# Optimization experiments

Measured on AMD Instinct MI355X. Metric: run time of the kernel, lower is better.

Reference implementation:

```python
import jax, jax.numpy as jnp
import numpy as np

H = 16      # num_heads
D = 64      # head_dim
HS = H * D  # hidden_size
B = 8
S = 1024


def setup_inputs() -> dict:
    key = jax.random.key(0)
    ks = jax.random.split(key, 12)
    scale = 1.0 / np.sqrt(HS)
    inp = {
        "v": jax.random.normal(ks[0], (B, S, HS), jnp.float32),
        "k": jax.random.normal(ks[1], (B, S, HS), jnp.float32),
        "q": jax.random.normal(ks[2], (B, S, HS), jnp.float32),
        "mask": jax.random.randint(ks[3], (B, 1, 1, S), 0, 2).astype(bool),
        "Wq": jax.random.normal(ks[4], (HS, HS), jnp.float32) * scale,
        "bq": jnp.zeros((HS,), jnp.float32),
        "Wk": jax.random.normal(ks[5], (HS, HS), jnp.float32) * scale,
        "bk": jnp.zeros((HS,), jnp.float32),
        "Wv": jax.random.normal(ks[6], (HS, HS), jnp.float32) * scale,
        "bv": jnp.zeros((HS,), jnp.float32),
        "Wo": jax.random.normal(ks[7], (HS, HS), jnp.float32) * scale,
        "bo": jnp.zeros((HS,), jnp.float32),
    }
    return inp


def _split_heads(x):
    b, s, _ = x.shape
    return x.reshape(b, s, H, D).transpose(0, 2, 1, 3)  # [B,H,S,D]


def reference(v, k, q, mask, Wq, bq, Wk, bk, Wv, bv, Wo, bo):
    # torch Linear: y = x @ W.T + b
    qh = _split_heads(q @ Wq.T + bq)
    kh = _split_heads(k @ Wk.T + bk)
    vh = _split_heads(v @ Wv.T + bv)
    scores = jnp.einsum("bhqd,bhkd->bhqk", qh, kh) / jnp.sqrt(jnp.float32(D))
    scores = jnp.where(mask, jnp.float32(-1e9), scores)
    att = jax.nn.softmax(scores, axis=-1)
    out = jnp.einsum("bhqk,bhkd->bhqd", att, vh)  # [B,H,S,D]
    out = out.transpose(0, 2, 1, 3).reshape(v.shape[0], -1, HS)
    return out @ Wo.T + bo
```

## Files before the change

### kernel.cpp

```cpp
#include <hip/hip_runtime.h>
#include <hip/hip_bf16.h>

#define HH   16
#define DD   64
#define HSZ  1024
#define BB   8
#define SS   1024
#define NTOK (BB*SS)
#define LOG2E 1.4426950408889634f
#define NCVTB 2048

typedef __attribute__((ext_vector_type(8))) short bf16x8;
typedef __attribute__((ext_vector_type(4))) float f32x4;
typedef unsigned short u16;
typedef __attribute__((ext_vector_type(4))) unsigned short u16x4;

__device__ __forceinline__ u16 bfc(float x) {
    __hip_bfloat16 h = __float2bfloat16(x);
    return *(u16*)&h;
}

__device__ __forceinline__ float exp2fast(float x) {
    return __builtin_amdgcn_exp2f(x);
}

__device__ __forceinline__ void gload16(const u16* g, u16* l) {
    __builtin_amdgcn_global_load_lds(
        (const __attribute__((address_space(1))) void*)g,
        (__attribute__((address_space(3))) void*)l, 16, 0, 0);
}

__device__ __forceinline__ void mask_scan_body(const void* mask,
                                               int* __restrict__ rmap,
                                               int* __restrict__ Larr, int b) {
    const int tid = threadIdx.x;
    const unsigned char* mball = (const unsigned char*)mask;

    __shared__ int fmt_s;
    __shared__ int wtot[4];
    __shared__ int Ls;
    if (tid == 0) fmt_s = 0;
    __syncthreads();
    int nz = 0;
    for (int i = tid; i < BB * SS; i += 256)
        if ((i & 3) && mball[i]) nz = 1;
    if (nz) fmt_s = 1;
    __syncthreads();
    const int fmt = fmt_s;

    const int base = tid * 4;
    int v[4];
#pragma unroll
    for (int e = 0; e < 4; ++e) {
        int val = fmt ? (int)mball[(size_t)b * SS + base + e]
                      : ((const int*)mask)[(size_t)b * SS + base + e];
        v[e] = (val == 0) ? 1 : 0;
    }
    int ts = v[0] + v[1] + v[2] + v[3];

    const int lane = tid & 63, wv = tid >> 6;
    int incl = ts;
#pragma unroll
    for (int d = 1; d < 64; d <<= 1) {
        int t = __shfl_up(incl, d);
        if (lane >= d) incl += t;
    }
    if (lane == 63) wtot[wv] = incl;
    __syncthreads();
    int woff = 0;
    for (int w = 0; w < wv; ++w) woff += wtot[w];
    int run = woff + incl - ts;
#pragma unroll
    for (int e = 0; e < 4; ++e) {
        if (v[e]) rmap[(size_t)b * SS + run] = base + e;
        run += v[e];
    }
    __syncthreads();
    if (tid == 0) {
        Ls = wtot[0] + wtot[1] + wtot[2] + wtot[3];
        Larr[b] = Ls;
    }
    __syncthreads();
    for (int j = Ls + tid; j < SS; j += 256) rmap[(size_t)b * SS + j] = 0;
}

__global__ __launch_bounds__(256) void cvt_scan_kernel(
        const float* __restrict__ q,  u16* __restrict__ dq,
        const float* __restrict__ k,  u16* __restrict__ dk,
        const float* __restrict__ v,  u16* __restrict__ dv,
        const float* __restrict__ w0, u16* __restrict__ dw0,
        const float* __restrict__ w1, u16* __restrict__ dw1,
        const float* __restrict__ w2, u16* __restrict__ dw2,
        const float* __restrict__ w3, u16* __restrict__ dw3,
        const void* mask, int* __restrict__ rmap, int* __restrict__ Larr) {
    if (blockIdx.x >= NCVTB) {
        mask_scan_body(mask, rmap, Larr, blockIdx.x - NCVTB);
        return;
    }
    const int NX = NTOK * HSZ / 8;
    const int NW = HSZ * HSZ / 8;
    const int ntot = 3 * NX + 4 * NW;
    int i = blockIdx.x * blockDim.x + threadIdx.x;
    const int stride = NCVTB * 256;
    for (; i < ntot; i += stride) {
        const float* s; u16* d; int j = i;
        if      (j < NX)            { s = q;  d = dq;  }
        else if ((j -= NX) < NX)    { s = k;  d = dk;  }
        else if ((j -= NX) < NX)    { s = v;  d = dv;  }
        else if ((j -= NX) < NW)    { s = w0; d = dw0; }
        else if ((j -= NW) < NW)    { s = w1; d = dw1; }
        else if ((j -= NW) < NW)    { s = w2; d = dw2; }
        else    { j -= NW;            s = w3; d = dw3; }
        f32x4 a = *(const f32x4*)&s[(size_t)j * 8];
        f32x4 b = *(const f32x4*)&s[(size_t)j * 8 + 4];
        union { bf16x8 v8; u16 u[8]; } t;
#pragma unroll
        for (int e = 0; e < 4; ++e) { t.u[e] = bfc(a[e]); t.u[4 + e] = bfc(b[e]); }
        *(bf16x8*)&d[(size_t)j * 8] = t.v8;
    }
}

template<int MODE>
__device__ __forceinline__ void proj_body(const u16* __restrict__ X,
                                          const u16* __restrict__ W,
                                          const float* __restrict__ bias,
                                          const int* __restrict__ rmap,
                                          const int* __restrict__ Larr,
                                          void* __restrict__ Yv,
                                          u16* Xs0, u16* Ws0,
                                          u16* Xs1, u16* Ws1) {
    const int bm = blockIdx.x;
    const int bn = blockIdx.y;
    const int tid  = threadIdx.x;
    const int wave = tid >> 6;
    const int lane = tid & 63;
    const int l15  = lane & 15;
    const int g    = lane >> 4;
    const int wr   = wave >> 1;
    const int wc   = wave & 1;

    const int b_   = bm >> 3;
    const int row0 = (bm & 7) * 128;
    if constexpr (MODE == 1 || MODE == 2) {
        const int L = Larr[b_];
        const int Lpad = ((L + 127) >> 7) << 7;
        if (row0 >= Lpad) return;
    }

    f32x4 acc[4][4] = {};

    int srow[4], scol[4], xr[4];
#pragma unroll
    for (int i = 0; i < 4; ++i) {
        const int slot = wave * 256 + i * 64 + lane;
        const int r = slot >> 3, s = slot & 7;
        srow[i] = r;
        scol[i] = (s ^ (r & 7)) * 8;
        if constexpr (MODE == 1 || MODE == 2)
            xr[i] = (b_ << 10) + rmap[(size_t)b_ * SS + row0 + r];
        else
            xr[i] = bm * 128 + r;
    }

    auto stage = [&](u16* Xd, u16* Wd, int k0) {
#pragma unroll
        for (int i = 0; i < 4; ++i) {
            gload16(&X[(size_t)xr[i] * HSZ + k0 + scol[i]], &Xd[(wave * 4 + i) * 512]);
            gload16(&W[(size_t)(bn * 128 + srow[i]) * HSZ + k0 + scol[i]],
                    &Wd[(wave * 4 + i) * 512]);
        }
    };
    auto compute = [&](const u16* Xc, const u16* Wc) {
#pragma unroll
        for (int kk = 0; kk < 2; ++kk) {
            const int cw = ((kk * 4 + g) ^ (l15 & 7)) * 8;
            bf16x8 a[4], bb[4];
#pragma unroll
            for (int m = 0; m < 4; ++m)
                a[m] = *(const bf16x8*)&Xc[(size_t)(wr * 64 + m * 16 + l15) * 64 + cw];
#pragma unroll
            for (int n = 0; n < 4; ++n)
                bb[n] = *(const bf16x8*)&Wc[(size_t)(wc * 64 + n * 16 + l15) * 64 + cw];
#pragma unroll
            for (int m = 0; m < 4; ++m)
#pragma unroll
                for (int n = 0; n < 4; ++n)
                    acc[m][n] = __builtin_amdgcn_mfma_f32_16x16x32_bf16(a[m], bb[n], acc[m][n], 0, 0, 0);
        }
    };

    stage(Xs0, Ws0, 0);
    __syncthreads();
    const int NT = HSZ / 64;
    for (int t = 0; t < NT; ++t) {
        const int p = t & 1;
        if (t + 1 < NT) stage(p ? Xs0 : Xs1, p ? Ws0 : Ws1, (t + 1) * 64);
        compute(p ? Xs1 : Xs0, p ? Ws1 : Ws0);
        __syncthreads();
    }

#pragma unroll
    for (int m = 0; m < 4; ++m) {
#pragma unroll
        for (int n = 0; n < 4; ++n) {
            const int o = bn * 128 + wc * 64 + n * 16 + l15;
            const float bvv = bias[o];
            const int h_ = o >> 6, d = o & 63;
#pragma unroll
            for (int r = 0; r < 4; ++r) {
                const int lrow = wr * 64 + m * 16 + g * 4 + r;
                float y = acc[m][n][r] + bvv;
                if constexpr (MODE == 0) {
                    const int nrow = bm * 128 + lrow;
                    int bb_ = nrow >> 10, s = nrow & 1023;
                    ((u16*)Yv)[(((size_t)bb_ * HH + h_) * SS + s) * DD + d] = bfc(y * (0.125f * LOG2E));
                } else if constexpr (MODE == 1) {
                    ((u16*)Yv)[(((size_t)b_ * HH + h_) * SS + row0 + lrow) * DD + d] = bfc(y);
                } else if constexpr (MODE == 2) {
                    ((u16*)Yv)[(((size_t)b_ * HH + h_) * DD + d) * SS + row0 + lrow] = bfc(y);
                } else {
                    const int nrow = bm * 128 + lrow;
                    ((float*)Yv)[(size_t)nrow * HSZ + o] = y;
                }
            }
        }
    }
}

__global__ __launch_bounds__(256) void proj_qkv_kernel(
        const u16* __restrict__ qbf, const u16* __restrict__ wqb,
        const float* __restrict__ bq, u16* __restrict__ Qh,
        const u16* __restrict__ kbf, const u16* __restrict__ wkb,
        const float* __restrict__ bk, u16* __restrict__ Kh,
        const u16* __restrict__ vbf, const u16* __restrict__ wvb,
        const float* __restrict__ bv, u16* __restrict__ Vt,
        const int* __restrict__ rmap, const int* __restrict__ Larr) {
    __shared__ u16 Xs0[128 * 64], Ws0[128 * 64];
    __shared__ u16 Xs1[128 * 64], Ws1[128 * 64];
    if (blockIdx.z == 0)
        proj_body<0>(qbf, wqb, bq, rmap, Larr, Qh, Xs0, Ws0, Xs1, Ws1);
    else if (blockIdx.z == 1)
        proj_body<1>(kbf, wkb, bk, rmap, Larr, Kh, Xs0, Ws0, Xs1, Ws1);
    else
        proj_body<2>(vbf, wvb, bv, rmap, Larr, Vt, Xs0, Ws0, Xs1, Ws1);
}

__global__ __launch_bounds__(256) void proj_o_kernel(
        const u16* __restrict__ X, const u16* __restrict__ W,
        const float* __restrict__ bias, const int* __restrict__ rmap,
        const int* __restrict__ Larr, float* __restrict__ out) {
    __shared__ u16 Xs0[128 * 64], Ws0[128 * 64];
    __shared__ u16 Xs1[128 * 64], Ws1[128 * 64];
    proj_body<3>(X, W, bias, rmap, Larr, out, Xs0, Ws0, Xs1, Ws1);
}

__global__ __launch_bounds__(256, 2) void attn_kernel(const u16* __restrict__ Qh,
                                                      const u16* __restrict__ Kh,
                                                      const u16* __restrict__ Vt,
                                                      const int* __restrict__ Larr,
                                                      u16* __restrict__ ctx) {
    const int qt = blockIdx.x;
    const int h  = blockIdx.y;
    const int b  = blockIdx.z;
    const int bh = b * HH + h;

    const int tid  = threadIdx.x;
    const int wave = tid >> 6;
    const int lane = tid & 63;
    const int l15  = lane & 15;
    const int g    = lane >> 4;
    const int qw0  = qt * 256 + wave * 64;

    __shared__ u16 Ks[2][64 * 64];
    __shared__ u16 Vs[2][64 * 64];
    __shared__ u16 Pw[4][2][16][72];

    const u16* Qb = Qh + ((size_t)bh * SS + qw0) * DD;
    const u16* Kb = Kh + (size_t)bh * SS * DD;
    const u16* Vb = Vt + (size_t)bh * DD * SS;

    const int L = Larr[b];
    const int nchunks = (L + 63) >> 6;

    bf16x8 qf[4][2];
#pragma unroll
    for (int qq = 0; qq < 4; ++qq)
#pragma unroll
        for (int hh = 0; hh < 2; ++hh)
            qf[qq][hh] = *(const bf16x8*)&Qb[(size_t)(qq * 16 + l15) * DD + hh * 32 + g * 8];

    f32x4 o[4][4] = {};
    float mrun[4] = { -3e38f, -3e38f, -3e38f, -3e38f };
    float lrun[4] = { 0.0f, 0.0f, 0.0f, 0.0f };

    auto stage = [&](u16* Kp, u16* Vp, int c0) {
#pragma unroll
        for (int i = 0; i < 2; ++i) {
            const int slot = i * 256 + tid;
            const int r  = slot >> 3;
            const int cs = ((slot & 7) ^ (r & 7)) * 8;
            u16* dstK = Kp + (size_t)(i * 256 + wave * 64) * 8;
            u16* dstV = Vp + (size_t)(i * 256 + wave * 64) * 8;
            gload16(&Kb[(size_t)(c0 + r) * DD + cs], dstK);
            gload16(&Vb[(size_t)r * SS + c0 + cs],   dstV);
        }
    };
    auto loadKfrag = [&](const u16* Kp, bf16x8 (&kf)[8]) {
#pragma unroll
        for (int kt = 0; kt < 4; ++kt)
#pragma unroll
            for (int hh = 0; hh < 2; ++hh) {
                const int cw = ((hh * 4 + g) ^ (l15 & 7)) * 8;
                kf[kt * 2 + hh] = *(const bf16x8*)&Kp[(size_t)(kt * 16 + l15) * 64 + cw];
            }
    };
    auto loadVfrag = [&](const u16* Vp, bf16x8 (&vf)[8]) {
#pragma unroll
        for (int dt = 0; dt < 4; ++dt)
#pragma unroll
            for (int kh = 0; kh < 2; ++kh) {
                const int cw = ((kh * 4 + g) ^ (l15 & 7)) * 8;
                vf[dt * 2 + kh] = *(const bf16x8*)&Vp[(size_t)(dt * 16 + l15) * 64 + cw];
            }
    };

    auto process = [&](const bf16x8 (&kf)[8], const bf16x8 (&vf)[8], int c0) {
#pragma unroll
        for (int qq = 0; qq < 4; ++qq) {
            f32x4 s[4];
#pragma unroll
            for (int kt = 0; kt < 4; ++kt) {
                f32x4 a = {};
                a = __builtin_amdgcn_mfma_f32_16x16x32_bf16(kf[kt * 2 + 0], qf[qq][0], a, 0, 0, 0);
                a = __builtin_amdgcn_mfma_f32_16x16x32_bf16(kf[kt * 2 + 1], qf[qq][1], a, 0, 0, 0);
                s[kt] = a;
            }
            if (c0 + 64 > L) {
#pragma unroll
                for (int kt = 0; kt < 4; ++kt) {
                    const int kid = c0 + kt * 16 + g * 4;
#pragma unroll
                    for (int r = 0; r < 4; ++r)
                        s[kt][r] = (kid + r < L) ? s[kt][r] : -3e38f;
                }
            }
            float pmk[4];
#pragma unroll
            for (int kt = 0; kt < 4; ++kt)
                pmk[kt] = fmaxf(fmaxf(s[kt][0], s[kt][1]), fmaxf(s[kt][2], s[kt][3]));
            float pm = fmaxf(fmaxf(pmk[0], pmk[1]), fmaxf(pmk[2], pmk[3]));
            pm = fmaxf(pm, __shfl_xor(pm, 16));
            pm = fmaxf(pm, __shfl_xor(pm, 32));

            if (!__all(pm <= mrun[qq] + 11.5416f)) {
                float sc = exp2fast(mrun[qq] - pm);
                mrun[qq] = pm;
                lrun[qq] *= sc;
                float f0 = __shfl(sc, g * 4 + 0);
                float f1 = __shfl(sc, g * 4 + 1);
                float f2 = __shfl(sc, g * 4 + 2);
                float f3 = __shfl(sc, g * 4 + 3);
#pragma unroll
                for (int dt = 0; dt < 4; ++dt) {
                    o[qq][dt][0] *= f0; o[qq][dt][1] *= f1;
                    o[qq][dt][2] *= f2; o[qq][dt][3] *= f3;
                }
            }

            float ls = 0.0f;
#pragma unroll
            for (int kt = 0; kt < 4; ++kt) {
                union { u16x4 v; u16 u[4]; } pv;
#pragma unroll
                for (int r = 0; r < 4; ++r) {
                    float e = exp2fast(s[kt][r] - mrun[qq]);
                    ls += e;
                    pv.u[r] = bfc(e);
                }
                *(u16x4*)&Pw[wave][qq & 1][l15][kt * 16 + g * 4] = pv.v;
            }
            ls += __shfl_xor(ls, 16);
            ls += __shfl_xor(ls, 32);
            lrun[qq] += ls;

#pragma unroll
            for (int kh = 0; kh < 2; ++kh) {
                bf16x8 pa = *(const bf16x8*)&Pw[wave][qq & 1][l15][kh * 32 + g * 8];
#pragma unroll
                for (int dt = 0; dt < 4; ++dt)
                    o[qq][dt] = __builtin_amdgcn_mfma_f32_16x16x32_bf16(pa, vf[dt * 2 + kh], o[qq][dt], 0, 0, 0);
            }
        }
    };

    stage(&Ks[0][0], &Vs[0][0], 0);
    __syncthreads();
    for (int c = 0; c < nchunks; ++c) {
        const int p = c & 1;
        if (c + 1 < nchunks) stage(&Ks[p ^ 1][0], &Vs[p ^ 1][0], (c + 1) * 64);
        bf16x8 kf[8], vf[8];
        loadKfrag(&Ks[p][0], kf);
        loadVfrag(&Vs[p][0], vf);
        process(kf, vf, c * 64);
        __syncthreads();
    }

#pragma unroll
    for (int qq = 0; qq < 4; ++qq) {
        float inv = 1.0f / lrun[qq];
        float i0 = __shfl(inv, g * 4 + 0);
        float i1 = __shfl(inv, g * 4 + 1);
        float i2 = __shfl(inv, g * 4 + 2);
        float i3 = __shfl(inv, g * 4 + 3);
#pragma unroll
        for (int dt = 0; dt < 4; ++dt) {
            const int col = h * DD + dt * 16 + l15;
            const int qr  = b * SS + qw0 + qq * 16 + g * 4;
            ctx[(size_t)(qr + 0) * HSZ + col] = bfc(o[qq][dt][0] * i0);
            ctx[(size_t)(qr + 1) * HSZ + col] = bfc(o[qq][dt][1] * i1);
            ctx[(size_t)(qr + 2) * HSZ + col] = bfc(o[qq][dt][2] * i2);
            ctx[(size_t)(qr + 3) * HSZ + col] = bfc(o[qq][dt][3] * i3);
        }
    }
}

extern "C" void kernel_launch(void* const* d_in, const int* in_sizes, int n_in,
                              void* d_out, int out_size, void* d_ws, size_t ws_size,
                              hipStream_t stream) {
    const float* v    = (const float*)d_in[0];
    const float* k    = (const float*)d_in[1];
    const float* q    = (const float*)d_in[2];
    const void*  mask = d_in[3];
    const float* Wq = (const float*)d_in[4];
    const float* bq = (const float*)d_in[5];
    const float* Wk = (const float*)d_in[6];
    const float* bk = (const float*)d_in[7];
    const float* Wv = (const float*)d_in[8];
    const float* bv = (const float*)d_in[9];
    const float* Wo = (const float*)d_in[10];
    const float* bo = (const float*)d_in[11];

    u16* qbf = (u16*)d_out;
    u16* kbf = qbf + (size_t)NTOK * HSZ;

    char* ws = (char*)d_ws;
    int*   rmap = (int*)ws;
    int*   Larr = (int*)(ws + 32768);
    u16*   wqb  = (u16*)(ws + 65536);
    u16*   wkb  = wqb + (size_t)HSZ * HSZ;
    u16*   wvb  = wkb + (size_t)HSZ * HSZ;
    u16*   wob  = wvb + (size_t)HSZ * HSZ;
    u16*   vbf  = wob + (size_t)HSZ * HSZ;
    u16*   Qh   = vbf + (size_t)NTOK * HSZ;
    u16*   Kh   = Qh + (size_t)NTOK * HSZ;
    u16*   Vt   = Kh + (size_t)NTOK * HSZ;
    u16*   ctx  = vbf;

    cvt_scan_kernel<<<NCVTB + BB, 256, 0, stream>>>(q, qbf, k, kbf, v, vbf,
                                                    Wq, wqb, Wk, wkb, Wv, wvb, Wo, wob,
                                                    mask, rmap, Larr);

    dim3 pgrid(NTOK / 128, HSZ / 128, 3);
    proj_qkv_kernel<<<pgrid, 256, 0, stream>>>(qbf, wqb, bq, Qh,
                                               kbf, wkb, bk, Kh,
                                               vbf, wvb, bv, Vt,
                                               rmap, Larr);

    dim3 agrid(SS / 256, HH, BB);
    attn_kernel<<<agrid, 256, 0, stream>>>(Qh, Kh, Vt, Larr, ctx);

    dim3 ogrid(NTOK / 128, HSZ / 128);
    proj_o_kernel<<<ogrid, 256, 0, stream>>>(ctx, wob, bo, rmap, Larr, (float*)d_out);
}
```

Baseline: 158.0 us.

## Shrink projection GEMM K-tile to 32 with paired-row swizzled LDS layout

The projection GEMM now stages 32-wide K slices instead of 64. Each pair of rows is packed into one 64-element LDS row with an XOR swizzle, and the fragment loads are remapped to match. This halves LDS use per block, which may let more blocks share a CU and hide latency. In exchange there are twice as many pipeline iterations and barriers per tile, and fewer MFMAs between each sync.

```diff
diff --git a/kernel.cpp b/kernel.cpp
--- a/kernel.cpp
+++ b/kernel.cpp
@@ -149,52 +149,54 @@
 
     f32x4 acc[4][4] = {};
 
-    int srow[4], scol[4], xr[4];
-#pragma unroll
-    for (int i = 0; i < 4; ++i) {
-        const int slot = wave * 256 + i * 64 + lane;
-        const int r = slot >> 3, s = slot & 7;
-        srow[i] = r;
-        scol[i] = (s ^ (r & 7)) * 8;
+    int xrow[2], wrow[2], scol[2];
+#pragma unroll
+    for (int i = 0; i < 2; ++i) {
+        const int slot = wave * 128 + i * 64 + lane;
+        const int sr = slot >> 3, qs = slot & 7;
+        const int p  = qs ^ (sr & 7);
+        const int r  = 2 * sr + (p >> 2);
+        scol[i] = (p & 3) * 8;
+        wrow[i] = bn * 128 + r;
         if constexpr (MODE == 1 || MODE == 2)
-            xr[i] = (b_ << 10) + rmap[(size_t)b_ * SS + row0 + r];
+            xrow[i] = (b_ << 10) + rmap[(size_t)b_ * SS + row0 + r];
         else
-            xr[i] = bm * 128 + r;
+            xrow[i] = bm * 128 + r;
     }
 
     auto stage = [&](u16* Xd, u16* Wd, int k0) {
 #pragma unroll
-        for (int i = 0; i < 4; ++i) {
-            gload16(&X[(size_t)xr[i] * HSZ + k0 + scol[i]], &Xd[(wave * 4 + i) * 512]);
-            gload16(&W[(size_t)(bn * 128 + srow[i]) * HSZ + k0 + scol[i]],
-                    &Wd[(wave * 4 + i) * 512]);
+        for (int i = 0; i < 2; ++i) {
+            gload16(&X[(size_t)xrow[i] * HSZ + k0 + scol[i]], &Xd[(wave * 2 + i) * 512]);
+            gload16(&W[(size_t)wrow[i] * HSZ + k0 + scol[i]], &Wd[(wave * 2 + i) * 512]);
         }
     };
     auto compute = [&](const u16* Xc, const u16* Wc) {
-#pragma unroll
-        for (int kk = 0; kk < 2; ++kk) {
-            const int cw = ((kk * 4 + g) ^ (l15 & 7)) * 8;
-            bf16x8 a[4], bb[4];
-#pragma unroll
-            for (int m = 0; m < 4; ++m)
-                a[m] = *(const bf16x8*)&Xc[(size_t)(wr * 64 + m * 16 + l15) * 64 + cw];
+        const int qoff = ((((l15 & 1) << 2) + g) ^ (l15 >> 1)) * 8;
+        bf16x8 a[4], bb[4];
+#pragma unroll
+        for (int m = 0; m < 4; ++m) {
+            const int sr = wr * 32 + m * 8 + (l15 >> 1);
+            a[m] = *(const bf16x8*)&Xc[(size_t)sr * 64 + qoff];
+        }
+#pragma unroll
+        for (int n = 0; n < 4; ++n) {
+            const int sr = wc * 32 + n * 8 + (l15 >> 1);
+            bb[n] = *(const bf16x8*)&Wc[(size_t)sr * 64 + qoff];
+        }
+#pragma unroll
+        for (int m = 0; m < 4; ++m)
 #pragma unroll
             for (int n = 0; n < 4; ++n)
-                bb[n] = *(const bf16x8*)&Wc[(size_t)(wc * 64 + n * 16 + l15) * 64 + cw];
-#pragma unroll
-            for (int m = 0; m < 4; ++m)
-#pragma unroll
-                for (int n = 0; n < 4; ++n)
-                    acc[m][n] = __builtin_amdgcn_mfma_f32_16x16x32_bf16(a[m], bb[n], acc[m][n], 0, 0, 0);
-        }
+                acc[m][n] = __builtin_amdgcn_mfma_f32_16x16x32_bf16(a[m], bb[n], acc[m][n], 0, 0, 0);
     };
 
     stage(Xs0, Ws0, 0);
     __syncthreads();
-    const int NT = HSZ / 64;
+    const int NT = HSZ / 32;
     for (int t = 0; t < NT; ++t) {
         const int p = t & 1;
-        if (t + 1 < NT) stage(p ? Xs0 : Xs1, p ? Ws0 : Ws1, (t + 1) * 64);
+        if (t + 1 < NT) stage(p ? Xs0 : Xs1, p ? Ws0 : Ws1, (t + 1) * 32);
         compute(p ? Xs1 : Xs0, p ? Ws1 : Ws0);
         __syncthreads();
     }
@@ -235,8 +237,8 @@
         const u16* __restrict__ vbf, const u16* __restrict__ wvb,
         const float* __restrict__ bv, u16* __restrict__ Vt,
         const int* __restrict__ rmap, const int* __restrict__ Larr) {
-    __shared__ u16 Xs0[128 * 64], Ws0[128 * 64];
-    __shared__ u16 Xs1[128 * 64], Ws1[128 * 64];
+    __shared__ u16 Xs0[128 * 32], Ws0[128 * 32];
+    __shared__ u16 Xs1[128 * 32], Ws1[128 * 32];
     if (blockIdx.z == 0)
         proj_body<0>(qbf, wqb, bq, rmap, Larr, Qh, Xs0, Ws0, Xs1, Ws1);
     else if (blockIdx.z == 1)
@@ -249,8 +251,8 @@
         const u16* __restrict__ X, const u16* __restrict__ W,
         const float* __restrict__ bias, const int* __restrict__ rmap,
         const int* __restrict__ Larr, float* __restrict__ out) {
-    __shared__ u16 Xs0[128 * 64], Ws0[128 * 64];
-    __shared__ u16 Xs1[128 * 64], Ws1[128 * 64];
+    __shared__ u16 Xs0[128 * 32], Ws0[128 * 32];
+    __shared__ u16 Xs1[128 * 32], Ws1[128 * 32];
     proj_body<3>(X, W, bias, rmap, Larr, out, Xs0, Ws0, Xs1, Ws1);
 }
 
```

New measurement: 176.1 us. +11.5%, slower.
